# Optimization experiments

Measured on AMD Instinct MI355X. Metric: run time of the kernel, lower is better.

## Reference

```python
import jax, jax.numpy as jnp
import numpy as np
from jax import lax


def conv3(x, w):
    # standard 3x3 conv, stride 1, pad 1, no bias (offset-predicting conv)
    return lax.conv_general_dilated(x, w, window_strides=(1, 1),
                                    padding=((1, 1), (1, 1)),
                                    dimension_numbers=('NCHW', 'OIHW', 'NCHW'))


def deform_conv(x, offset, weight, bias, groups):
    # torchvision.ops.DeformConv2d semantics, kernel 3x3, stride 1, pad 1,
    # dilation 1, conv groups == offset groups == `groups`.
    B, C, H, W = x.shape
    kH = kW = 3
    K = kH * kW
    pad = 1
    G = groups
    Cg = C // G
    outC = weight.shape[0]
    outCg = outC // G
    # offset layout: [B, G, K, 2(y,x), H, W]
    off = offset.reshape(B, G, K, 2, H, W)
    ky, kx = jnp.meshgrid(jnp.arange(kH, dtype=x.dtype),
                          jnp.arange(kW, dtype=x.dtype), indexing='ij')
    kyf = ky.reshape(K)
    kxf = kx.reshape(K)
    hg = jnp.arange(H, dtype=x.dtype) - pad
    wg = jnp.arange(W, dtype=x.dtype) - pad
    # sampling positions [B, G, K, H, W]
    py = off[:, :, :, 0] + hg[None, None, None, :, None] + kyf[None, None, :, None, None]
    px = off[:, :, :, 1] + wg[None, None, None, None, :] + kxf[None, None, :, None, None]
    y0 = jnp.floor(py)
    x0 = jnp.floor(px)
    wy = py - y0
    wx = px - x0
    xf = x.reshape(B, G, Cg, H * W)

    def gather(iy, ix):
        # bilinear corner gather with implicit zero padding
        valid = ((iy >= 0) & (iy < H) & (ix >= 0) & (ix < W)).astype(x.dtype)
        iyc = jnp.clip(iy, 0, H - 1).astype(jnp.int32)
        ixc = jnp.clip(ix, 0, W - 1).astype(jnp.int32)
        idx = (iyc * W + ixc).reshape(B, G, 1, K * H * W)
        idx = jnp.broadcast_to(idx, (B, G, Cg, K * H * W))
        v = jnp.take_along_axis(xf, idx, axis=3).reshape(B, G, Cg, K, H, W)
        return v * valid[:, :, None]

    one = jnp.asarray(1, x.dtype)
    val = ((one - wy) * (one - wx))[:, :, None] * gather(y0, x0) \
        + ((one - wy) * wx)[:, :, None] * gather(y0, x0 + 1) \
        + (wy * (one - wx))[:, :, None] * gather(y0 + 1, x0) \
        + (wy * wx)[:, :, None] * gather(y0 + 1, x0 + 1)
    # grouped conv as einsum over (Cg, K)
    wgrp = weight.reshape(G, outCg, Cg, K)
    out = jnp.einsum('bgckhw,gock->bgohw', val, wgrp).reshape(B, outC, H, W)
    return out + bias[None, :, None, None]


def setup_inputs() -> dict:
    key = jax.random.key(0)
    ks = jax.random.split(key, 16)
    B, C, H, W = 8, 64, 96, 96
    s = 0.01  # keep predicted offsets small / numerically tame
    fr = jax.random.normal(ks[0], (B, C, H, W), jnp.float32)
    ft = jax.random.normal(ks[1], (B, C, H, W), jnp.float32)
    # block 1: inC=128, 4 groups -> offset channels 72, deform weight [64, 32, 3, 3]
    off1_w = jax.random.normal(ks[2], (72, 128, 3, 3), jnp.float32) * s
    def1_w = jax.random.normal(ks[3], (64, 32, 3, 3), jnp.float32) * s
    def1_b = jax.random.normal(ks[4], (64,), jnp.float32) * s
    # blocks 2,3: inC=64, 4 groups
    off2_w = jax.random.normal(ks[5], (72, 64, 3, 3), jnp.float32) * s
    def2_w = jax.random.normal(ks[6], (64, 16, 3, 3), jnp.float32) * s
    def2_b = jax.random.normal(ks[7], (64,), jnp.float32) * s
    off3_w = jax.random.normal(ks[8], (72, 64, 3, 3), jnp.float32) * s
    def3_w = jax.random.normal(ks[9], (64, 16, 3, 3), jnp.float32) * s
    def3_b = jax.random.normal(ks[10], (64,), jnp.float32) * s
    # block 4: inC=64, 2 groups -> offset channels 36, deform weight [64, 32, 3, 3]
    off4_w = jax.random.normal(ks[11], (36, 64, 3, 3), jnp.float32) * s
    def4_w = jax.random.normal(ks[12], (64, 32, 3, 3), jnp.float32) * s
    def4_b = jax.random.normal(ks[13], (64,), jnp.float32) * s
    return {"fr": fr, "ft": ft,
            "off1_w": off1_w, "def1_w": def1_w, "def1_b": def1_b,
            "off2_w": off2_w, "def2_w": def2_w, "def2_b": def2_b,
            "off3_w": off3_w, "def3_w": def3_w, "def3_b": def3_b,
            "off4_w": off4_w, "def4_w": def4_w, "def4_b": def4_b}


def reference(fr, ft, off1_w, def1_w, def1_b, off2_w, def2_w, def2_b,
              off3_w, def3_w, def3_b, off4_w, def4_w, def4_b):
    cat_feat = jnp.concatenate((fr, ft), axis=1)            # [B, 2C, H, W]
    feat1 = deform_conv(cat_feat, conv3(cat_feat, off1_w), def1_w, def1_b, 4)
    feat2 = deform_conv(feat1, conv3(feat1, off2_w), def2_w, def2_b, 4)
    feat3 = deform_conv(feat2, conv3(feat2, off3_w), def3_w, def3_b, 4)
    # block 4: offsets predicted from feat3, sampling applied to ft
    aligned = deform_conv(ft, conv3(feat3, off4_w), def4_w, def4_b, 2)
    return aligned
```

## Files before the change

kernel.cpp:

```cpp
#include <hip/hip_runtime.h>
#include <hip/hip_bf16.h>


#define HH 96
#define WW 96
#define HWSZ (HH * WW)
#define BB 8
#define PW 98
#define PP (PW * PW)

using bf16x8 = __attribute__((ext_vector_type(8))) short;
using f32x4  = __attribute__((ext_vector_type(4))) float;

__device__ __forceinline__ unsigned int f2bf(float f) {
    __hip_bfloat16 h = __float2bfloat16(f);
    return (unsigned int)*reinterpret_cast<unsigned short*>(&h);
}
__device__ __forceinline__ float bf2f(unsigned short u) {
    return __uint_as_float(((unsigned int)u) << 16);
}

__global__ void prepack_w_kernel(const float* __restrict__ w, short* __restrict__ wp,
                                 int outC, int C, int MT, int KS) {
    int i = blockIdx.x * 256 + threadIdx.x;
    if (i >= MT * KS * 64) return;
    int lane = i & 63;
    int s = (i >> 6) % KS;
    int m = (i >> 6) / KS;
    int oc = m * 16 + (lane & 15);
    short v[8];
#pragma unroll
    for (int j = 0; j < 8; ++j) {
        int k = s * 32 + (lane >> 4) * 8 + j;
        int t = k / C, c = k % C;
        float f = (oc < outC) ? w[((size_t)oc * C + c) * 9 + t] : 0.f;
        v[j] = (short)f2bf(f);
    }
    *reinterpret_cast<bf16x8*>(wp + (size_t)i * 8) = *reinterpret_cast<bf16x8*>(v);
}

__global__ void pad_nhwc64_kernel(const float* __restrict__ src,
                                  __hip_bfloat16* __restrict__ out) {
    int i = blockIdx.x * 256 + threadIdx.x;
    if (i >= BB * PP) return;
    int px = i % PW, py = (i / PW) % PW, b = i / PP;
    unsigned int* op = reinterpret_cast<unsigned int*>(out + (size_t)i * 64);
    if (px == 0 || px == PW - 1 || py == 0 || py == PW - 1) {
#pragma unroll
        for (int c = 0; c < 32; ++c) op[c] = 0u;
        return;
    }
    const float* sp = src + (size_t)b * 64 * HWSZ + (py - 1) * WW + (px - 1);
#pragma unroll 8
    for (int c = 0; c < 32; ++c)
        op[c] = f2bf(sp[(size_t)(2 * c) * HWSZ]) | (f2bf(sp[(size_t)(2 * c + 1) * HWSZ]) << 16);
}

__global__ void zero_border64_kernel(__hip_bfloat16* __restrict__ p) {
    int i = blockIdx.x * 256 + threadIdx.x;
    if (i >= BB * PP) return;
    int px = i % PW, py = (i / PW) % PW;
    if (px == 0 || px == PW - 1 || py == 0 || py == PW - 1) {
        unsigned int* q = reinterpret_cast<unsigned int*>(p + (size_t)i * 64);
#pragma unroll
        for (int c = 0; c < 32; ++c) q[c] = 0u;
    }
}

template <int C>
__global__ __launch_bounds__(256) void conv3_mfma_kernel(
    const __hip_bfloat16* __restrict__ xa,
    const __hip_bfloat16* __restrict__ xb,
    const short* __restrict__ wp,
    __hip_bfloat16* __restrict__ offb, int outC) {
    constexpr int KS = 9 * C / 32;
    int lane = threadIdx.x & 63;
    int wave = threadIdx.x >> 6;
    int y = blockIdx.x * 4 + wave;
    int m = blockIdx.y;
    int b = blockIdx.z;
    int l15 = lane & 15, lhi = lane >> 4;

    f32x4 acc[6];
#pragma unroll
    for (int nt = 0; nt < 6; ++nt) acc[nt] = (f32x4){0.f, 0.f, 0.f, 0.f};

    const short* wpm = wp + ((size_t)m * KS) * 64 * 8 + (size_t)lane * 8;

#pragma unroll 3
    for (int s = 0; s < KS; ++s) {
        bf16x8 afrag = *reinterpret_cast<const bf16x8*>(wpm + (size_t)s * 64 * 8);
        int t  = (s * 32) / C;
        int cb = (s * 32) % C;
        const __hip_bfloat16* xp = (cb < 64) ? xa : xb;
        int c0 = (cb & 63) + lhi * 8;
        int ky = t / 3, kx = t % 3;
        const short* bbase = reinterpret_cast<const short*>(xp)
            + (((size_t)b * PW + (y + ky)) * PW + kx + l15) * 64 + c0;
#pragma unroll
        for (int nt = 0; nt < 6; ++nt) {
            bf16x8 bfrag = *reinterpret_cast<const bf16x8*>(bbase + (size_t)nt * 16 * 64);
            acc[nt] = __builtin_amdgcn_mfma_f32_16x16x32_bf16(afrag, bfrag, acc[nt], 0, 0, 0);
        }
    }

    int ocb = m * 16 + lhi * 4;
#pragma unroll
    for (int nt = 0; nt < 6; ++nt) {
        int pix = y * WW + nt * 16 + l15;
#pragma unroll
        for (int r = 0; r < 4; ++r) {
            int oc = ocb + r;
            if (oc < outC) {
                unsigned short hv = (unsigned short)f2bf(acc[nt][r]);
                *reinterpret_cast<unsigned short*>(
                    offb + ((size_t)b * outC + oc) * HWSZ + pix) = hv;
            }
        }
    }
}

template <int CG, int OCG, int OFFC, bool SRCBF, bool HASN, bool HASH, bool FINAL>
__global__ __launch_bounds__(256) void deform4_kernel(
    const void* __restrict__ xA, const void* __restrict__ xB,
    const __hip_bfloat16* __restrict__ offb,
    const float* __restrict__ w,
    const float* __restrict__ bias,
    __hip_bfloat16* __restrict__ anchw,
    __hip_bfloat16* __restrict__ fnhwc,
    float* __restrict__ outp) {
    int pix = blockIdx.x * 256 + threadIdx.x;
    int g   = blockIdx.y;
    int b   = blockIdx.z;
    int x = pix % WW, y = pix / WW;

    const __hip_bfloat16* ob = offb + ((size_t)b * OFFC + g * 18) * HWSZ + pix;

    float bw0[9], bw1[9], bw2[9], bw3[9];
    int   bi0[9], bi1[9], bi2[9], bi3[9];
#pragma unroll
    for (int k = 0; k < 9; ++k) {
        int ky = k / 3, kx = k % 3;
        float offy = bf2f(*reinterpret_cast<const unsigned short*>(ob + (size_t)(2 * k) * HWSZ));
        float offx = bf2f(*reinterpret_cast<const unsigned short*>(ob + (size_t)(2 * k + 1) * HWSZ));
        float py = offy + (float)(y - 1 + ky);
        float px = offx + (float)(x - 1 + kx);
        float fy0 = floorf(py), fx0 = floorf(px);
        float wy = py - fy0, wx = px - fx0;
        int y0 = (int)fy0, x0 = (int)fx0;
        int y1 = y0 + 1,  x1 = x0 + 1;
        bool vy0 = (y0 >= 0) && (y0 < HH);
        bool vy1 = (y1 >= 0) && (y1 < HH);
        bool vx0 = (x0 >= 0) && (x0 < WW);
        bool vx1 = (x1 >= 0) && (x1 < WW);
        int cy0 = min(max(y0, 0), HH - 1), cy1 = min(max(y1, 0), HH - 1);
        int cx0 = min(max(x0, 0), WW - 1), cx1 = min(max(x1, 0), WW - 1);
        bw0[k] = (1.f - wy) * (1.f - wx) * ((vy0 && vx0) ? 1.f : 0.f);
        bw1[k] = (1.f - wy) * wx         * ((vy0 && vx1) ? 1.f : 0.f);
        bw2[k] = wy * (1.f - wx)         * ((vy1 && vx0) ? 1.f : 0.f);
        bw3[k] = wy * wx                 * ((vy1 && vx1) ? 1.f : 0.f);
        bi0[k] = cy0 * WW + cx0;  bi1[k] = cy0 * WW + cx1;
        bi2[k] = cy1 * WW + cx0;  bi3[k] = cy1 * WW + cx1;
    }

    float acc[OCG];
#pragma unroll
    for (int o = 0; o < OCG; ++o) acc[o] = bias[g * OCG + o];

    int gc = g * CG;
    const void* srcv = (gc < 64) ? xA : xB;
    size_t pbase = (size_t)b * 64 + (size_t)((gc < 64) ? gc : gc - 64);

    for (int c = 0; c < CG; ++c) {
        float v[9];
        if constexpr (SRCBF) {
            const unsigned short* p = (const unsigned short*)srcv + (pbase + c) * HWSZ;
#pragma unroll
            for (int k = 0; k < 9; ++k)
                v[k] = bw0[k] * bf2f(p[bi0[k]]) + bw1[k] * bf2f(p[bi1[k]])
                     + bw2[k] * bf2f(p[bi2[k]]) + bw3[k] * bf2f(p[bi3[k]]);
        } else {
            const float* p = (const float*)srcv + (pbase + c) * HWSZ;
#pragma unroll
            for (int k = 0; k < 9; ++k)
                v[k] = bw0[k] * p[bi0[k]] + bw1[k] * p[bi1[k]]
                     + bw2[k] * p[bi2[k]] + bw3[k] * p[bi3[k]];
        }
        const float* wc = w + ((size_t)(g * OCG) * CG + c) * 9;
#pragma unroll
        for (int o = 0; o < OCG; ++o) {
            const float* wo = wc + (size_t)o * CG * 9;
#pragma unroll
            for (int k = 0; k < 9; ++k) acc[o] = fmaf(v[k], wo[k], acc[o]);
        }
    }

    if constexpr (HASN) {
#pragma unroll
        for (int o = 0; o < OCG; ++o)
            *reinterpret_cast<unsigned short*>(
                anchw + ((size_t)b * 64 + g * OCG + o) * HWSZ + pix) =
                (unsigned short)f2bf(acc[o]);
    }
    if constexpr (HASH) {
        unsigned int* q = reinterpret_cast<unsigned int*>(
            fnhwc + (((size_t)b * PW + (y + 1)) * PW + (x + 1)) * 64 + g * OCG);
#pragma unroll
        for (int o = 0; o < OCG / 2; ++o)
            q[o] = f2bf(acc[2 * o]) | (f2bf(acc[2 * o + 1]) << 16);
    }
    if constexpr (FINAL) {
        float* op = outp + ((size_t)b * 64 + g * OCG) * HWSZ + pix;
#pragma unroll
        for (int o = 0; o < OCG; ++o) op[(size_t)o * HWSZ] = acc[o];
    }
}

extern "C" void kernel_launch(void* const* d_in, const int* in_sizes, int n_in,
                              void* d_out, int out_size, void* d_ws, size_t ws_size,
                              hipStream_t stream) {
    const float* fr     = (const float*)d_in[0];
    const float* ft     = (const float*)d_in[1];
    const float* off1_w = (const float*)d_in[2];
    const float* def1_w = (const float*)d_in[3];
    const float* def1_b = (const float*)d_in[4];
    const float* off2_w = (const float*)d_in[5];
    const float* def2_w = (const float*)d_in[6];
    const float* def2_b = (const float*)d_in[7];
    const float* off3_w = (const float*)d_in[8];
    const float* def3_w = (const float*)d_in[9];
    const float* def3_b = (const float*)d_in[10];
    const float* off4_w = (const float*)d_in[11];
    const float* def4_w = (const float*)d_in[12];
    const float* def4_b = (const float*)d_in[13];
    float* outp = (float*)d_out;

    char* ws = (char*)d_ws;
    const size_t offb_sz = (size_t)BB * 72 * HWSZ * 2;
    const size_t pbuf_sz = (size_t)BB * PP * 64 * 2;
    __hip_bfloat16* offb = (__hip_bfloat16*)ws; ws += offb_sz;
    __hip_bfloat16* P0   = (__hip_bfloat16*)ws; ws += pbuf_sz;
    __hip_bfloat16* P1   = (__hip_bfloat16*)ws; ws += pbuf_sz;
    __hip_bfloat16* P2   = (__hip_bfloat16*)ws; ws += pbuf_sz;
    __hip_bfloat16* P3   = (__hip_bfloat16*)ws; ws += pbuf_sz;
    short* wp1 = (short*)ws; ws += (size_t)5 * 36 * 64 * 8 * 2;
    short* wp2 = (short*)ws; ws += (size_t)5 * 18 * 64 * 8 * 2;
    short* wp3 = (short*)ws; ws += (size_t)5 * 18 * 64 * 8 * 2;
    short* wp4 = (short*)ws; ws += (size_t)3 * 18 * 64 * 8 * 2;

    dim3 blk(256);
    int padBlocks = (BB * PP + 255) / 256;

    prepack_w_kernel<<<(5 * 36 * 64 + 255) / 256, blk, 0, stream>>>(off1_w, wp1, 72, 128, 5, 36);
    prepack_w_kernel<<<(5 * 18 * 64 + 255) / 256, blk, 0, stream>>>(off2_w, wp2, 72, 64, 5, 18);
    prepack_w_kernel<<<(5 * 18 * 64 + 255) / 256, blk, 0, stream>>>(off3_w, wp3, 72, 64, 5, 18);
    prepack_w_kernel<<<(3 * 18 * 64 + 255) / 256, blk, 0, stream>>>(off4_w, wp4, 36, 64, 3, 18);

    pad_nhwc64_kernel<<<padBlocks, blk, 0, stream>>>(fr, P0);
    pad_nhwc64_kernel<<<padBlocks, blk, 0, stream>>>(ft, P1);
    zero_border64_kernel<<<padBlocks, blk, 0, stream>>>(P2);

    dim3 gDefG4(36, 4, BB), gDefG2(36, 2, BB);

    conv3_mfma_kernel<128><<<dim3(24, 5, BB), blk, 0, stream>>>(P0, P1, wp1, offb, 72);
    deform4_kernel<32, 16, 72, false, true, true, false><<<gDefG4, blk, 0, stream>>>(
        fr, ft, offb, def1_w, def1_b, P3 , P2 , nullptr);

    conv3_mfma_kernel<64><<<dim3(24, 5, BB), blk, 0, stream>>>(P2, P2, wp2, offb, 72);
    deform4_kernel<16, 16, 72, true, true, true, false><<<gDefG4, blk, 0, stream>>>(
        P3, P3, offb, def2_w, def2_b, P1 , P0 , nullptr);

    conv3_mfma_kernel<64><<<dim3(24, 5, BB), blk, 0, stream>>>(P0, P0, wp3, offb, 72);
    deform4_kernel<16, 16, 72, true, false, true, false><<<gDefG4, blk, 0, stream>>>(
        P1, P1, offb, def3_w, def3_b, nullptr, P2 , nullptr);

    conv3_mfma_kernel<64><<<dim3(24, 3, BB), blk, 0, stream>>>(P2, P2, wp4, offb, 36);
    deform4_kernel<32, 32, 36, false, false, false, true><<<gDefG2, blk, 0, stream>>>(
        ft, ft, offb, def4_w, def4_b, nullptr, nullptr, outp);
}
```

Baseline: 1.101 ms.

## Store offsets in fp32 and split padded NHWC writes into separate pad kernels

The deform kernel no longer writes a padded NHWC copy of its output directly. It writes only NCHW bf16, and a new padA kernel transposes that into the padded NHWC buffer before each offset conv. The offset tensor is now stored as fp32 instead of bf16, which doubles its traffic but keeps offset precision. This adds three launches and an extra read/write pass, with fewer workspace buffers in exchange.

Measured after the change: 1.125 ms. +2.1%, slower.

```diff
diff --git a/kernel.cpp b/kernel.cpp
--- a/kernel.cpp
+++ b/kernel.cpp
@@ -56,15 +56,23 @@
         op[c] = f2bf(sp[(size_t)(2 * c) * HWSZ]) | (f2bf(sp[(size_t)(2 * c + 1) * HWSZ]) << 16);
 }
 
-__global__ void zero_border64_kernel(__hip_bfloat16* __restrict__ p) {
+__global__ void padA_kernel(const __hip_bfloat16* __restrict__ src,
+                            __hip_bfloat16* __restrict__ out) {
     int i = blockIdx.x * 256 + threadIdx.x;
     if (i >= BB * PP) return;
-    int px = i % PW, py = (i / PW) % PW;
+    int px = i % PW, py = (i / PW) % PW, b = i / PP;
+    unsigned int* op = reinterpret_cast<unsigned int*>(out + (size_t)i * 64);
     if (px == 0 || px == PW - 1 || py == 0 || py == PW - 1) {
-        unsigned int* q = reinterpret_cast<unsigned int*>(p + (size_t)i * 64);
-#pragma unroll
-        for (int c = 0; c < 32; ++c) q[c] = 0u;
-    }
+#pragma unroll
+        for (int c = 0; c < 32; ++c) op[c] = 0u;
+        return;
+    }
+    const unsigned short* sp = reinterpret_cast<const unsigned short*>(src)
+        + (size_t)b * 64 * HWSZ + (py - 1) * WW + (px - 1);
+#pragma unroll 8
+    for (int c = 0; c < 32; ++c)
+        op[c] = (unsigned int)sp[(size_t)(2 * c) * HWSZ]
+              | ((unsigned int)sp[(size_t)(2 * c + 1) * HWSZ] << 16);
 }
 
 template <int C>
@@ -72,7 +80,7 @@
     const __hip_bfloat16* __restrict__ xa,
     const __hip_bfloat16* __restrict__ xb,
     const short* __restrict__ wp,
-    __hip_bfloat16* __restrict__ offb, int outC) {
+    float* __restrict__ offb, int outC) {
     constexpr int KS = 9 * C / 32;
     int lane = threadIdx.x & 63;
     int wave = threadIdx.x >> 6;
@@ -111,38 +119,34 @@
 #pragma unroll
         for (int r = 0; r < 4; ++r) {
             int oc = ocb + r;
-            if (oc < outC) {
-                unsigned short hv = (unsigned short)f2bf(acc[nt][r]);
-                *reinterpret_cast<unsigned short*>(
-                    offb + ((size_t)b * outC + oc) * HWSZ + pix) = hv;
-            }
-        }
-    }
-}
-
-template <int CG, int OCG, int OFFC, bool SRCBF, bool HASN, bool HASH, bool FINAL>
-__global__ __launch_bounds__(256) void deform4_kernel(
+            if (oc < outC)
+                offb[((size_t)b * outC + oc) * HWSZ + pix] = acc[nt][r];
+        }
+    }
+}
+
+template <int CG, int OCG, int OFFC, bool SRCBF, bool DSTBF>
+__global__ __launch_bounds__(256) void deform5_kernel(
     const void* __restrict__ xA, const void* __restrict__ xB,
-    const __hip_bfloat16* __restrict__ offb,
+    const float* __restrict__ offb,
     const float* __restrict__ w,
     const float* __restrict__ bias,
     __hip_bfloat16* __restrict__ anchw,
-    __hip_bfloat16* __restrict__ fnhwc,
     float* __restrict__ outp) {
     int pix = blockIdx.x * 256 + threadIdx.x;
     int g   = blockIdx.y;
     int b   = blockIdx.z;
     int x = pix % WW, y = pix / WW;
 
-    const __hip_bfloat16* ob = offb + ((size_t)b * OFFC + g * 18) * HWSZ + pix;
+    const float* offp = offb + ((size_t)b * OFFC + g * 18) * HWSZ + pix;
 
     float bw0[9], bw1[9], bw2[9], bw3[9];
     int   bi0[9], bi1[9], bi2[9], bi3[9];
 #pragma unroll
     for (int k = 0; k < 9; ++k) {
         int ky = k / 3, kx = k % 3;
-        float offy = bf2f(*reinterpret_cast<const unsigned short*>(ob + (size_t)(2 * k) * HWSZ));
-        float offx = bf2f(*reinterpret_cast<const unsigned short*>(ob + (size_t)(2 * k + 1) * HWSZ));
+        float offy = offp[(size_t)(2 * k + 0) * HWSZ];
+        float offx = offp[(size_t)(2 * k + 1) * HWSZ];
         float py = offy + (float)(y - 1 + ky);
         float px = offx + (float)(x - 1 + kx);
         float fy0 = floorf(py), fx0 = floorf(px);
@@ -195,21 +199,13 @@
         }
     }
 
-    if constexpr (HASN) {
+    if constexpr (DSTBF) {
 #pragma unroll
         for (int o = 0; o < OCG; ++o)
             *reinterpret_cast<unsigned short*>(
                 anchw + ((size_t)b * 64 + g * OCG + o) * HWSZ + pix) =
                 (unsigned short)f2bf(acc[o]);
-    }
-    if constexpr (HASH) {
-        unsigned int* q = reinterpret_cast<unsigned int*>(
-            fnhwc + (((size_t)b * PW + (y + 1)) * PW + (x + 1)) * 64 + g * OCG);
-#pragma unroll
-        for (int o = 0; o < OCG / 2; ++o)
-            q[o] = f2bf(acc[2 * o]) | (f2bf(acc[2 * o + 1]) << 16);
-    }
-    if constexpr (FINAL) {
+    } else {
         float* op = outp + ((size_t)b * 64 + g * OCG) * HWSZ + pix;
 #pragma unroll
         for (int o = 0; o < OCG; ++o) op[(size_t)o * HWSZ] = acc[o];
@@ -236,17 +232,18 @@
     float* outp = (float*)d_out;
 
     char* ws = (char*)d_ws;
-    const size_t offb_sz = (size_t)BB * 72 * HWSZ * 2;
-    const size_t pbuf_sz = (size_t)BB * PP * 64 * 2;
-    __hip_bfloat16* offb = (__hip_bfloat16*)ws; ws += offb_sz;
-    __hip_bfloat16* P0   = (__hip_bfloat16*)ws; ws += pbuf_sz;
-    __hip_bfloat16* P1   = (__hip_bfloat16*)ws; ws += pbuf_sz;
-    __hip_bfloat16* P2   = (__hip_bfloat16*)ws; ws += pbuf_sz;
-    __hip_bfloat16* P3   = (__hip_bfloat16*)ws; ws += pbuf_sz;
+    const size_t offb_sz = (size_t)BB * 72 * HWSZ * 4;
+    const size_t a_sz    = (size_t)BB * 64 * HWSZ * 2;
+    const size_t p_sz    = (size_t)BB * PP * 64 * 2;
+    float*          offb = (float*)ws;          ws += offb_sz;
+    __hip_bfloat16* A1   = (__hip_bfloat16*)ws; ws += a_sz;
+    __hip_bfloat16* P0   = (__hip_bfloat16*)ws; ws += p_sz;
+    __hip_bfloat16* P1   = (__hip_bfloat16*)ws; ws += p_sz;
     short* wp1 = (short*)ws; ws += (size_t)5 * 36 * 64 * 8 * 2;
     short* wp2 = (short*)ws; ws += (size_t)5 * 18 * 64 * 8 * 2;
     short* wp3 = (short*)ws; ws += (size_t)5 * 18 * 64 * 8 * 2;
     short* wp4 = (short*)ws; ws += (size_t)3 * 18 * 64 * 8 * 2;
+    __hip_bfloat16* A2 = P1;
 
     dim3 blk(256);
     int padBlocks = (BB * PP + 255) / 256;
@@ -258,23 +255,25 @@
 
     pad_nhwc64_kernel<<<padBlocks, blk, 0, stream>>>(fr, P0);
     pad_nhwc64_kernel<<<padBlocks, blk, 0, stream>>>(ft, P1);
-    zero_border64_kernel<<<padBlocks, blk, 0, stream>>>(P2);
 
     dim3 gDefG4(36, 4, BB), gDefG2(36, 2, BB);
 
     conv3_mfma_kernel<128><<<dim3(24, 5, BB), blk, 0, stream>>>(P0, P1, wp1, offb, 72);
-    deform4_kernel<32, 16, 72, false, true, true, false><<<gDefG4, blk, 0, stream>>>(
-        fr, ft, offb, def1_w, def1_b, P3 , P2 , nullptr);
-
-    conv3_mfma_kernel<64><<<dim3(24, 5, BB), blk, 0, stream>>>(P2, P2, wp2, offb, 72);
-    deform4_kernel<16, 16, 72, true, true, true, false><<<gDefG4, blk, 0, stream>>>(
-        P3, P3, offb, def2_w, def2_b, P1 , P0 , nullptr);
-
+    deform5_kernel<32, 16, 72, false, true><<<gDefG4, blk, 0, stream>>>(
+        fr, ft, offb, def1_w, def1_b, A1, nullptr);
+
+    padA_kernel<<<padBlocks, blk, 0, stream>>>(A1, P0);
+    conv3_mfma_kernel<64><<<dim3(24, 5, BB), blk, 0, stream>>>(P0, P0, wp2, offb, 72);
+    deform5_kernel<16, 16, 72, true, true><<<gDefG4, blk, 0, stream>>>(
+        A1, A1, offb, def2_w, def2_b, A2, nullptr);
+
+    padA_kernel<<<padBlocks, blk, 0, stream>>>(A2, P0);
     conv3_mfma_kernel<64><<<dim3(24, 5, BB), blk, 0, stream>>>(P0, P0, wp3, offb, 72);
-    deform4_kernel<16, 16, 72, true, false, true, false><<<gDefG4, blk, 0, stream>>>(
-        P1, P1, offb, def3_w, def3_b, nullptr, P2 , nullptr);
-
-    conv3_mfma_kernel<64><<<dim3(24, 3, BB), blk, 0, stream>>>(P2, P2, wp4, offb, 36);
-    deform4_kernel<32, 32, 36, false, false, false, true><<<gDefG2, blk, 0, stream>>>(
-        ft, ft, offb, def4_w, def4_b, nullptr, nullptr, outp);
-}
+    deform5_kernel<16, 16, 72, true, true><<<gDefG4, blk, 0, stream>>>(
+        A2, A2, offb, def3_w, def3_b, A1, nullptr);
+
+    padA_kernel<<<padBlocks, blk, 0, stream>>>(A1, P0);
+    conv3_mfma_kernel<64><<<dim3(24, 3, BB), blk, 0, stream>>>(P0, P0, wp4, offb, 36);
+    deform5_kernel<32, 32, 36, false, false><<<gDefG2, blk, 0, stream>>>(
+        ft, ft, offb, def4_w, def4_b, nullptr, outp);
+}
```
